# Performance work log

Measured on AMD Instinct MI355X. Metric: run time of the kernel, lower is better.

Reference implementation:

```python
import jax, jax.numpy as jnp
import numpy as np

H, N, DH, DO = 4, 4096, 128, 128   # heads, nodes, dim_hid, dim_out
ALPHA = 0.2                        # leaky-relu negative slope
NEG = -9e15                        # mask fill value (as in pyGAT)


def setup_inputs() -> dict:
    key = jax.random.key(0)
    ks = jax.random.split(key, 6)
    chems = jax.random.normal(ks[0], (H, N, DH), jnp.float32)
    adj = jax.random.randint(ks[1], (N, N), 0, 2, jnp.int32)
    s1 = 1.0 / np.sqrt(DH)
    W1 = jax.random.uniform(ks[2], (H, DH, DH), jnp.float32, -s1, s1)
    a1 = jax.random.uniform(ks[3], (H, 2 * DH), jnp.float32, -s1, s1)
    s2 = 1.0 / np.sqrt(DO)
    W2 = jax.random.uniform(ks[4], (H, H * DH, DO), jnp.float32, -s2, s2)
    a2 = jax.random.uniform(ks[5], (H, 2 * DO), jnp.float32, -s2, s2)
    return {"chems": chems, "adj": adj, "W1": W1, "a1": a1, "W2": W2, "a2": a2}


def _gat(h, W, a, mask):
    # Dense GAT layer (pyGAT style), concat=True -> elu output.
    Wh = h @ W                       # [N, d]
    d = W.shape[-1]
    src = Wh @ a[:d]                 # [N] contribution of row node
    dst = Wh @ a[d:]                 # [N] contribution of col node
    e = jax.nn.leaky_relu(src[:, None] + dst[None, :], negative_slope=ALPHA)  # [N, N]
    e = jnp.where(mask, e, NEG)
    att = jax.nn.softmax(e, axis=-1)
    return jax.nn.elu(att @ Wh)      # [N, d]


def reference(chems, adj, W1, a1, W2, a2):
    mask = adj > 0
    # stage 1: one uniform GAT head per chems[i], concat along features
    x1 = jax.vmap(_gat, in_axes=(0, 0, 0, None))(chems, W1, a1, mask)  # [H, N, DH]
    x = jnp.transpose(x1, (1, 0, 2)).reshape(N, H * DH)                # [N, H*DH]
    # stage 2: H output heads on shared x, concat along features
    x2 = jax.vmap(_gat, in_axes=(None, 0, 0, None))(x, W2, a2, mask)   # [H, N, DO]
    return jnp.transpose(x2, (1, 0, 2)).reshape(N, H * DO)             # [N, H*DO]
```

## Files before the change

### kernel.cpp

```cpp
#include <hip/hip_runtime.h>
#include <hip/hip_bf16.h>

typedef unsigned long long ull;
typedef __attribute__((ext_vector_type(8))) short short8;
typedef __attribute__((ext_vector_type(8))) unsigned short us8;
typedef __attribute__((ext_vector_type(4))) unsigned short us4;
typedef __attribute__((ext_vector_type(4))) float f32x4;

constexpr int NN = 4096;
constexpr int HH = 4;
constexpr int DD = 128;
constexpr int NW = 64;
constexpr int JSPLIT = 4;
constexpr float L2E = 1.44269504088896f;

__device__ inline unsigned short f2bf(float x) {
  unsigned u = __float_as_uint(x);
  u += 0x7FFFu + ((u >> 16) & 1u);
  return (unsigned short)(u >> 16);
}

__device__ inline short fbf(float x) {
  __bf16 b = (__bf16)x;
  short r;
  __builtin_memcpy(&r, &b, 2);
  return r;
}

__device__ inline void gload16(const void* g, void* l) {
  __builtin_amdgcn_global_load_lds(
      (const __attribute__((address_space(1))) unsigned int*)g,
      (__attribute__((address_space(3))) unsigned int*)l, 16, 0, 0);
}

__global__ __launch_bounds__(256) void pack_mask_kernel(const int* __restrict__ adj,
                                                        ull* __restrict__ mbT) {
  const int i    = blockIdx.x;
  const int lane = threadIdx.x & 63;
  const int wave = threadIdx.x >> 6;
  for (int w = wave; w < NW; w += 4) {
    int v = adj[(size_t)i * NN + w * 64 + lane];
    ull m = __ballot(v > 0);
    if (lane == 0) mbT[(size_t)w * NN + i] = m;
  }
}

__global__ __launch_bounds__(256) void cvt_bf16_kernel(const float* __restrict__ in,
                                                       unsigned short* __restrict__ out,
                                                       int n8) {
  int i = blockIdx.x * 256 + threadIdx.x;
  if (i >= n8) return;
  f32x4 a = *(const f32x4*)(in + i * 8);
  f32x4 b = *(const f32x4*)(in + i * 8 + 4);
  us8 v;
#pragma unroll
  for (int q = 0; q < 4; ++q) { v[q] = f2bf(a[q]); v[q + 4] = f2bf(b[q]); }
  *(us8*)(out + i * 8) = v;
}

__global__ __launch_bounds__(256) void prep_w_kernel(const float* __restrict__ W,
                                                     unsigned short* __restrict__ WT,
                                                     int KT) {
  int id = blockIdx.x * 256 + threadIdx.x;
  int total = HH * KT * 128 * 8;
  if (id >= total) return;
  int kc = id & 7;
  int c  = (id >> 3) & 127;
  int kt = (id >> 10) % KT;
  int h  = id / (KT * 1024);
  int K  = KT * 64;
  const float* src = W + ((size_t)h * K + kt * 64 + kc * 8) * 128 + c;
  us8 v;
#pragma unroll
  for (int e = 0; e < 8; ++e) v[e] = f2bf(src[(size_t)e * 128]);
  *(us8*)(WT + (((size_t)(h * KT + kt) * 128 + c) * 64 + ((kc ^ (c & 7)) * 8))) = v;
}

__global__ __launch_bounds__(512) void gemm_mfma_kernel(
    const unsigned short* __restrict__ A, int sA, long hsA,
    const unsigned short* __restrict__ WT, int KT,
    unsigned short* __restrict__ WhT, const float* __restrict__ avec,
    float* __restrict__ srcO, float* __restrict__ dstO) {
  __shared__ unsigned short Al[2][64 * 64];
  __shared__ unsigned short Wl[2][128 * 64];
  __shared__ float sdred[2][64][2];
  const int t   = threadIdx.x;
  const int h   = blockIdx.y;
  const int i0  = blockIdx.x * 64;
  const int l   = t & 63;
  const int wv  = t >> 6;
  const int l15 = l & 15;
  const int l16 = l >> 4;
  const int wr  = (wv >> 1) * 16;
  const int wc  = (wv & 1) * 64;
  const unsigned short* Ab = A + (size_t)h * hsA;
  const unsigned short* Wb = WT + (size_t)h * KT * 8192;

  const int arowA = wv * 8 + (l >> 3);
  const int agA   = l & 7;

  f32x4 acc[4];
#pragma unroll
  for (int cf = 0; cf < 4; ++cf) acc[cf] = (f32x4){0.f, 0.f, 0.f, 0.f};

#define G_STAGE(kt_, b_)                                                          \
  {                                                                               \
    gload16(Ab + (size_t)(i0 + arowA) * sA + (kt_) * 64 + ((agA ^ (arowA & 7)) * 8), \
            &Al[b_][(wv * 64) * 8]);                                              \
    const unsigned short* wt = Wb + (size_t)(kt_)*8192;                           \
    gload16(wt + (size_t)(wv * 64 + l) * 8, &Wl[b_][(wv * 64) * 8]);              \
    gload16(wt + (size_t)(512 + wv * 64 + l) * 8, &Wl[b_][(512 + wv * 64) * 8]);  \
  }

  G_STAGE(0, 0);
  __syncthreads();
  int buf = 0;
  for (int kt = 0; kt < KT; ++kt) {
    if (kt + 1 < KT) G_STAGE(kt + 1, buf ^ 1);
    const int arow = wr + l15;
#pragma unroll
    for (int s = 0; s < 2; ++s) {
      int kc = s * 4 + l16;
      short8 a = *(const short8*)&Al[buf][arow * 64 + ((kc ^ (arow & 7)) * 8)];
#pragma unroll
      for (int cf = 0; cf < 4; ++cf) {
        int c = wc + cf * 16 + l15;
        short8 b = *(const short8*)&Wl[buf][c * 64 + ((kc ^ (c & 7)) * 8)];
        acc[cf] = __builtin_amdgcn_mfma_f32_16x16x32_bf16(a, b, acc[cf], 0, 0, 0);
      }
    }
    __syncthreads();
    buf ^= 1;
  }

  const int wblk = i0 >> 6;
  const int g    = (wr >> 3) + (l16 >> 1);
  const int eoff = (l16 * 4) & 7;
#pragma unroll
  for (int cf = 0; cf < 4; ++cf) {
    int c = wc + cf * 16 + l15;
    us4 pk;
#pragma unroll
    for (int r = 0; r < 4; ++r) pk[r] = f2bf(acc[cf][r]);
    *(us4*)(WhT + (((size_t)(h * 64 + wblk) * 128 + c) * 64 + ((g ^ (c & 7)) * 8) + eoff)) = pk;
  }

  float ps[4] = {0.f, 0.f, 0.f, 0.f}, pd[4] = {0.f, 0.f, 0.f, 0.f};
#pragma unroll
  for (int cf = 0; cf < 4; ++cf) {
    int c = wc + cf * 16 + l15;
    float as = avec[h * 2 * DD + c];
    float ad = avec[h * 2 * DD + DD + c];
#pragma unroll
    for (int r = 0; r < 4; ++r) { ps[r] += acc[cf][r] * as; pd[r] += acc[cf][r] * ad; }
  }
#pragma unroll
  for (int off = 1; off < 16; off <<= 1) {
#pragma unroll
    for (int r = 0; r < 4; ++r) {
      ps[r] += __shfl_xor(ps[r], off, 64);
      pd[r] += __shfl_xor(pd[r], off, 64);
    }
  }
  if (l15 == 0) {
#pragma unroll
    for (int r = 0; r < 4; ++r) {
      sdred[wv & 1][wr + l16 * 4 + r][0] = ps[r];
      sdred[wv & 1][wr + l16 * 4 + r][1] = pd[r];
    }
  }
  __syncthreads();
  if (t < 128) {
    int row = t >> 1, sel = t & 1;
    float v = (sdred[0][row][sel] + sdred[1][row][sel]) * L2E;
    (sel ? dstO : srcO)[(h << 12) + i0 + row] = v;
  }
#undef G_STAGE
}

__global__ __launch_bounds__(256) void att_part_kernel(
    const unsigned short* __restrict__ WhT, const float* __restrict__ sL,
    const float* __restrict__ dL, const ull* __restrict__ mbT,
    float* __restrict__ part, float* __restrict__ sums) {
  __shared__ unsigned short whl[2][128 * 64];
  const int t   = threadIdx.x;
  const int h   = blockIdx.y;
  const int jq  = blockIdx.x & (JSPLIT - 1);
  const int i0  = (blockIdx.x / JSPLIT) * 64;
  const int l   = t & 63;
  const int wv  = t >> 6;
  const int l15 = l & 15;
  const int l16 = l >> 4;
  const int wr  = wv * 16;
  const int NIT = NW / JSPLIT;

  const int arow  = i0 + wr + l15;
  const int gr    = (h << 12) + arow;
  const float s_i = sL[gr];
  const float* dj = dL + (h << 12);
  const unsigned short* Wt = WhT + (size_t)(h * 64) * 8192;
  const int w0 = jq * NIT;

  f32x4 acc[8];
#pragma unroll
  for (int cf = 0; cf < 8; ++cf) acc[cf] = (f32x4){0.f, 0.f, 0.f, 0.f};
  float psum = 0.f;

#define A_STAGE(w_, b_)                                                    \
  {                                                                        \
    const unsigned short* gt = Wt + (size_t)(w_)*8192;                     \
    gload16(gt + (size_t)(0 * 256 + t) * 8, &whl[b_][(0 * 256 + wv * 64) * 8]); \
    gload16(gt + (size_t)(1 * 256 + t) * 8, &whl[b_][(1 * 256 + wv * 64) * 8]); \
    gload16(gt + (size_t)(2 * 256 + t) * 8, &whl[b_][(2 * 256 + wv * 64) * 8]); \
    gload16(gt + (size_t)(3 * 256 + t) * 8, &whl[b_][(3 * 256 + wv * 64) * 8]); \
  }

  A_STAGE(w0, 0);
  __syncthreads();
  int buf = 0;
  for (int it = 0; it < NIT; ++it) {
    const int w = w0 + it;
    if (it + 1 < NIT) A_STAGE(w + 1, buf ^ 1);
    ull mb = mbT[(size_t)w * NN + arow];
    short8 afr[2];
#pragma unroll
    for (int s = 0; s < 2; ++s) {
      const int bsh = s * 32 + l16 * 8;
      f32x4 d0 = *(const f32x4*)(dj + w * 64 + bsh);
      f32x4 d1 = *(const f32x4*)(dj + w * 64 + bsh + 4);
      unsigned mb8 = (unsigned)((mb >> bsh) & 0xffull);
#pragma unroll
      for (int q = 0; q < 8; ++q) {
        float tt = s_i + ((q < 4) ? d0[q] : d1[q - 4]);
        float z = fmaxf(tt, 0.2f * tt);
        z = ((mb8 >> q) & 1u) ? z : -1.0e30f;
        float pf = __builtin_amdgcn_exp2f(z);
        psum += pf;
        afr[s][q] = fbf(pf);
      }
    }
    __builtin_amdgcn_s_setprio(1);
#pragma unroll
    for (int s = 0; s < 2; ++s) {
      int kc = s * 4 + l16;
#pragma unroll
      for (int cf = 0; cf < 8; ++cf) {
        int c = cf * 16 + l15;
        short8 b = *(const short8*)&whl[buf][c * 64 + ((kc ^ (c & 7)) * 8)];
        acc[cf] = __builtin_amdgcn_mfma_f32_16x16x32_bf16(afr[s], b, acc[cf], 0, 0, 0);
      }
    }
    __builtin_amdgcn_s_setprio(0);
    __syncthreads();
    buf ^= 1;
  }
  psum += __shfl_xor(psum, 16, 64);
  psum += __shfl_xor(psum, 32, 64);
  if (l16 == 0) sums[(size_t)jq * (HH * NN) + gr] = psum;
  float* pb = part + ((size_t)jq * (HH * NN) + (h << 12) + i0) * 128;
#pragma unroll
  for (int cf = 0; cf < 8; ++cf) {
#pragma unroll
    for (int r = 0; r < 4; ++r)
      pb[(size_t)(wr + l16 * 4 + r) * 128 + cf * 16 + l15] = acc[cf][r];
  }
#undef A_STAGE
}

template <int OUTBF>
__global__ __launch_bounds__(256) void fuse_kernel(const float* __restrict__ part,
                                                   const float* __restrict__ sums,
                                                   void* __restrict__ outp) {
  int idx = blockIdx.x * 256 + threadIdx.x;
  int c4 = (idx & 31) * 4;
  int g = idx >> 5;
  int node = g & (NN - 1), h = g >> 12;
  f32x4 a = (f32x4){0.f, 0.f, 0.f, 0.f};
  float den = 0.f;
#pragma unroll
  for (int q = 0; q < JSPLIT; ++q) {
    f32x4 v = *(const f32x4*)(part + ((size_t)q * (HH * NN) + g) * 128 + c4);
#pragma unroll
    for (int r = 0; r < 4; ++r) a[r] += v[r];
    den += sums[(size_t)q * (HH * NN) + g];
  }
  float inv = 1.0f / den;
  size_t o = (size_t)node * (HH * DD) + h * DD + c4;
#pragma unroll
  for (int r = 0; r < 4; ++r) {
    float v = a[r] * inv;
    a[r] = v > 0.f ? v : __expf(v) - 1.f;
  }
  if (OUTBF) {
    us4 pk;
#pragma unroll
    for (int r = 0; r < 4; ++r) pk[r] = (unsigned short)fbf(a[r]);
    *(us4*)((unsigned short*)outp + o) = pk;
  } else {
    *(f32x4*)((float*)outp + o) = a;
  }
}

extern "C" void kernel_launch(void* const* d_in, const int* in_sizes, int n_in,
                              void* d_out, int out_size, void* d_ws, size_t ws_size,
                              hipStream_t stream) {
  const float* chems = (const float*)d_in[0];
  const int*   adj   = (const int*)d_in[1];
  const float* W1    = (const float*)d_in[2];
  const float* a1    = (const float*)d_in[3];
  const float* W2    = (const float*)d_in[4];
  const float* a2    = (const float*)d_in[5];
  float* out = (float*)d_out;

  char* p = (char*)d_ws;
  auto alloc = [&](size_t bytes) { char* r = p; p += (bytes + 255) & ~255ull; return r; };
  ull*   mbT  = (ull*)alloc((size_t)NW * NN * 8);
  unsigned short* cbf  = (unsigned short*)alloc((size_t)HH * NN * DD * 2);
  unsigned short* xbf  = (unsigned short*)alloc((size_t)NN * HH * DD * 2);
  unsigned short* WhT1 = (unsigned short*)alloc((size_t)HH * 64 * 8192 * 2);
  unsigned short* WhT2 = (unsigned short*)alloc((size_t)HH * 64 * 8192 * 2);
  unsigned short* WT1  = (unsigned short*)alloc((size_t)HH * 2 * 8192 * 2);
  unsigned short* WT2  = (unsigned short*)alloc((size_t)HH * 8 * 8192 * 2);
  float* parts = (float*)alloc((size_t)JSPLIT * HH * NN * 128 * 4);
  float* sums  = (float*)alloc((size_t)JSPLIT * HH * NN * 4);
  float* src1 = (float*)alloc((size_t)HH * NN * 4);
  float* dst1 = (float*)alloc((size_t)HH * NN * 4);
  float* src2 = (float*)alloc((size_t)HH * NN * 4);
  float* dst2 = (float*)alloc((size_t)HH * NN * 4);
  (void)ws_size; (void)in_sizes; (void)n_in; (void)out_size;

  pack_mask_kernel<<<NN, 256, 0, stream>>>(adj, mbT);
  cvt_bf16_kernel<<<(HH * NN * DD / 8 + 255) / 256, 256, 0, stream>>>(chems, cbf,
                                                                      HH * NN * DD / 8);
  prep_w_kernel<<<(HH * 2 * 1024 + 255) / 256, 256, 0, stream>>>(W1, WT1, 2);
  prep_w_kernel<<<(HH * 8 * 1024 + 255) / 256, 256, 0, stream>>>(W2, WT2, 8);

  const int FUSE_BLK = (HH * NN * DD / 4) / 256;

  gemm_mfma_kernel<<<dim3(NN / 64, HH), 512, 0, stream>>>(
      cbf, DD, (long)NN * DD, WT1, 2, WhT1, a1, src1, dst1);
  att_part_kernel<<<dim3(JSPLIT * NN / 64, HH), 256, 0, stream>>>(
      WhT1, src1, dst1, mbT, parts, sums);
  fuse_kernel<1><<<FUSE_BLK, 256, 0, stream>>>(parts, sums, xbf);
  gemm_mfma_kernel<<<dim3(NN / 64, HH), 512, 0, stream>>>(
      xbf, HH * DD, 0L, WT2, 8, WhT2, a2, src2, dst2);
  att_part_kernel<<<dim3(JSPLIT * NN / 64, HH), 256, 0, stream>>>(
      WhT2, src2, dst2, mbT, parts, sums);
  fuse_kernel<0><<<FUSE_BLK, 256, 0, stream>>>(parts, sums, out);
}
```

Measured before the change: 228.6 us.

## Factor attention exponent into per-node exps and double rows per block

Uses exp2(lrelu(s+d)) = max(e^s·e^d, e^{0.2s}·e^{0.2d}), computing the per-node exponentials once in the projection GEMM epilogue. The attention kernel then needs only multiplies and a max per pair instead of a transcendental exp. Each block now covers 128 rows, so every warp does two 16-row MFMA tiles that share the staged Wh tile. JSPLIT is raised to 8 with launch bounds set for 4 blocks, which keeps the grid size unchanged but doubles the partial-sum buffers that fuse must read. Unnormalized products could overflow or lose precision for large scores, because no max is subtracted and the exponentials are not stabilized.

```diff
diff --git a/kernel.cpp b/kernel.cpp
--- a/kernel.cpp
+++ b/kernel.cpp
@@ -11,7 +11,7 @@
 constexpr int HH = 4;
 constexpr int DD = 128;
 constexpr int NW = 64;
-constexpr int JSPLIT = 4;
+constexpr int JSPLIT = 8;
 constexpr float L2E = 1.44269504088896f;
 
 __device__ inline unsigned short f2bf(float x) {
@@ -80,7 +80,8 @@
     const unsigned short* __restrict__ A, int sA, long hsA,
     const unsigned short* __restrict__ WT, int KT,
     unsigned short* __restrict__ WhT, const float* __restrict__ avec,
-    float* __restrict__ srcO, float* __restrict__ dstO) {
+    float* __restrict__ eS, float* __restrict__ eS2,
+    float* __restrict__ eD, float* __restrict__ eD2) {
   __shared__ unsigned short Al[2][64 * 64];
   __shared__ unsigned short Wl[2][128 * 64];
   __shared__ float sdred[2][64][2];
@@ -173,38 +174,48 @@
   if (t < 128) {
     int row = t >> 1, sel = t & 1;
     float v = (sdred[0][row][sel] + sdred[1][row][sel]) * L2E;
-    (sel ? dstO : srcO)[(h << 12) + i0 + row] = v;
+    float e1 = __builtin_amdgcn_exp2f(v);
+    float e2 = __builtin_amdgcn_exp2f(0.2f * v);
+    int gg = (h << 12) + i0 + row;
+    if (sel) { eD[gg] = e1; eD2[gg] = e2; }
+    else     { eS[gg] = e1; eS2[gg] = e2; }
   }
 #undef G_STAGE
 }
 
-__global__ __launch_bounds__(256) void att_part_kernel(
-    const unsigned short* __restrict__ WhT, const float* __restrict__ sL,
-    const float* __restrict__ dL, const ull* __restrict__ mbT,
+__global__ __launch_bounds__(256, 4) void att_part_kernel(
+    const unsigned short* __restrict__ WhT, const float* __restrict__ eS,
+    const float* __restrict__ eS2, const float* __restrict__ eD,
+    const float* __restrict__ eD2, const ull* __restrict__ mbT,
     float* __restrict__ part, float* __restrict__ sums) {
   __shared__ unsigned short whl[2][128 * 64];
   const int t   = threadIdx.x;
   const int h   = blockIdx.y;
   const int jq  = blockIdx.x & (JSPLIT - 1);
-  const int i0  = (blockIdx.x / JSPLIT) * 64;
+  const int i0  = (blockIdx.x / JSPLIT) * 128;
   const int l   = t & 63;
   const int wv  = t >> 6;
   const int l15 = l & 15;
   const int l16 = l >> 4;
-  const int wr  = wv * 16;
+  const int wr  = wv * 32;
   const int NIT = NW / JSPLIT;
 
-  const int arow  = i0 + wr + l15;
-  const int gr    = (h << 12) + arow;
-  const float s_i = sL[gr];
-  const float* dj = dL + (h << 12);
+  const int r0  = i0 + wr + l15;
+  const int g0  = (h << 12) + r0;
+  const float es0 = eS[g0],      es0b = eS2[g0];
+  const float es1 = eS[g0 + 16], es1b = eS2[g0 + 16];
+  const float* pD  = eD  + (h << 12);
+  const float* pD2 = eD2 + (h << 12);
   const unsigned short* Wt = WhT + (size_t)(h * 64) * 8192;
   const int w0 = jq * NIT;
 
-  f32x4 acc[8];
-#pragma unroll
-  for (int cf = 0; cf < 8; ++cf) acc[cf] = (f32x4){0.f, 0.f, 0.f, 0.f};
-  float psum = 0.f;
+  f32x4 acc0[8], acc1[8];
+#pragma unroll
+  for (int cf = 0; cf < 8; ++cf) {
+    acc0[cf] = (f32x4){0.f, 0.f, 0.f, 0.f};
+    acc1[cf] = (f32x4){0.f, 0.f, 0.f, 0.f};
+  }
+  float ps0 = 0.f, ps1 = 0.f;
 
 #define A_STAGE(w_, b_)                                                    \
   {                                                                        \
@@ -221,22 +232,30 @@
   for (int it = 0; it < NIT; ++it) {
     const int w = w0 + it;
     if (it + 1 < NIT) A_STAGE(w + 1, buf ^ 1);
-    ull mb = mbT[(size_t)w * NN + arow];
-    short8 afr[2];
+    ull mb0 = mbT[(size_t)w * NN + r0];
+    ull mb1 = mbT[(size_t)w * NN + r0 + 16];
+    short8 a0[2], a1[2];
 #pragma unroll
     for (int s = 0; s < 2; ++s) {
       const int bsh = s * 32 + l16 * 8;
-      f32x4 d0 = *(const f32x4*)(dj + w * 64 + bsh);
-      f32x4 d1 = *(const f32x4*)(dj + w * 64 + bsh + 4);
-      unsigned mb8 = (unsigned)((mb >> bsh) & 0xffull);
+      f32x4 dA  = *(const f32x4*)(pD  + w * 64 + bsh);
+      f32x4 dB  = *(const f32x4*)(pD  + w * 64 + bsh + 4);
+      f32x4 d2A = *(const f32x4*)(pD2 + w * 64 + bsh);
+      f32x4 d2B = *(const f32x4*)(pD2 + w * 64 + bsh + 4);
+      unsigned m0 = (unsigned)((mb0 >> bsh) & 0xffull);
+      unsigned m1 = (unsigned)((mb1 >> bsh) & 0xffull);
 #pragma unroll
       for (int q = 0; q < 8; ++q) {
-        float tt = s_i + ((q < 4) ? d0[q] : d1[q - 4]);
-        float z = fmaxf(tt, 0.2f * tt);
-        z = ((mb8 >> q) & 1u) ? z : -1.0e30f;
-        float pf = __builtin_amdgcn_exp2f(z);
-        psum += pf;
-        afr[s][q] = fbf(pf);
+        float ed  = (q < 4) ? dA[q] : dB[q - 4];
+        float ed2 = (q < 4) ? d2A[q] : d2B[q - 4];
+        float p0 = fmaxf(es0 * ed, es0b * ed2);
+        p0 = ((m0 >> q) & 1u) ? p0 : 0.f;
+        ps0 += p0;
+        a0[s][q] = fbf(p0);
+        float p1 = fmaxf(es1 * ed, es1b * ed2);
+        p1 = ((m1 >> q) & 1u) ? p1 : 0.f;
+        ps1 += p1;
+        a1[s][q] = fbf(p1);
       }
     }
     __builtin_amdgcn_s_setprio(1);
@@ -247,22 +266,30 @@
       for (int cf = 0; cf < 8; ++cf) {
         int c = cf * 16 + l15;
         short8 b = *(const short8*)&whl[buf][c * 64 + ((kc ^ (c & 7)) * 8)];
-        acc[cf] = __builtin_amdgcn_mfma_f32_16x16x32_bf16(afr[s], b, acc[cf], 0, 0, 0);
+        acc0[cf] = __builtin_amdgcn_mfma_f32_16x16x32_bf16(a0[s], b, acc0[cf], 0, 0, 0);
+        acc1[cf] = __builtin_amdgcn_mfma_f32_16x16x32_bf16(a1[s], b, acc1[cf], 0, 0, 0);
       }
     }
     __builtin_amdgcn_s_setprio(0);
     __syncthreads();
     buf ^= 1;
   }
-  psum += __shfl_xor(psum, 16, 64);
-  psum += __shfl_xor(psum, 32, 64);
-  if (l16 == 0) sums[(size_t)jq * (HH * NN) + gr] = psum;
+  ps0 += __shfl_xor(ps0, 16, 64);
+  ps0 += __shfl_xor(ps0, 32, 64);
+  ps1 += __shfl_xor(ps1, 16, 64);
+  ps1 += __shfl_xor(ps1, 32, 64);
+  if (l16 == 0) {
+    sums[(size_t)jq * (HH * NN) + g0] = ps0;
+    sums[(size_t)jq * (HH * NN) + g0 + 16] = ps1;
+  }
   float* pb = part + ((size_t)jq * (HH * NN) + (h << 12) + i0) * 128;
 #pragma unroll
   for (int cf = 0; cf < 8; ++cf) {
 #pragma unroll
-    for (int r = 0; r < 4; ++r)
-      pb[(size_t)(wr + l16 * 4 + r) * 128 + cf * 16 + l15] = acc[cf][r];
+    for (int r = 0; r < 4; ++r) {
+      pb[(size_t)(wr + l16 * 4 + r) * 128 + cf * 16 + l15] = acc0[cf][r];
+      pb[(size_t)(wr + 16 + l16 * 4 + r) * 128 + cf * 16 + l15] = acc1[cf][r];
+    }
   }
 #undef A_STAGE
 }
@@ -323,10 +350,14 @@
   unsigned short* WT2  = (unsigned short*)alloc((size_t)HH * 8 * 8192 * 2);
   float* parts = (float*)alloc((size_t)JSPLIT * HH * NN * 128 * 4);
   float* sums  = (float*)alloc((size_t)JSPLIT * HH * NN * 4);
-  float* src1 = (float*)alloc((size_t)HH * NN * 4);
-  float* dst1 = (float*)alloc((size_t)HH * NN * 4);
-  float* src2 = (float*)alloc((size_t)HH * NN * 4);
-  float* dst2 = (float*)alloc((size_t)HH * NN * 4);
+  float* eS1  = (float*)alloc((size_t)HH * NN * 4);
+  float* eS1b = (float*)alloc((size_t)HH * NN * 4);
+  float* eD1  = (float*)alloc((size_t)HH * NN * 4);
+  float* eD1b = (float*)alloc((size_t)HH * NN * 4);
+  float* eS2  = (float*)alloc((size_t)HH * NN * 4);
+  float* eS2b = (float*)alloc((size_t)HH * NN * 4);
+  float* eD2  = (float*)alloc((size_t)HH * NN * 4);
+  float* eD2b = (float*)alloc((size_t)HH * NN * 4);
   (void)ws_size; (void)in_sizes; (void)n_in; (void)out_size;
 
   pack_mask_kernel<<<NN, 256, 0, stream>>>(adj, mbT);
@@ -338,13 +369,13 @@
   const int FUSE_BLK = (HH * NN * DD / 4) / 256;
 
   gemm_mfma_kernel<<<dim3(NN / 64, HH), 512, 0, stream>>>(
-      cbf, DD, (long)NN * DD, WT1, 2, WhT1, a1, src1, dst1);
-  att_part_kernel<<<dim3(JSPLIT * NN / 64, HH), 256, 0, stream>>>(
-      WhT1, src1, dst1, mbT, parts, sums);
+      cbf, DD, (long)NN * DD, WT1, 2, WhT1, a1, eS1, eS1b, eD1, eD1b);
+  att_part_kernel<<<dim3(JSPLIT * NN / 128, HH), 256, 0, stream>>>(
+      WhT1, eS1, eS1b, eD1, eD1b, mbT, parts, sums);
   fuse_kernel<1><<<FUSE_BLK, 256, 0, stream>>>(parts, sums, xbf);
   gemm_mfma_kernel<<<dim3(NN / 64, HH), 512, 0, stream>>>(
-      xbf, HH * DD, 0L, WT2, 8, WhT2, a2, src2, dst2);
-  att_part_kernel<<<dim3(JSPLIT * NN / 64, HH), 256, 0, stream>>>(
-      WhT2, src2, dst2, mbT, parts, sums);
+      xbf, HH * DD, 0L, WT2, 8, WhT2, a2, eS2, eS2b, eD2, eD2b);
+  att_part_kernel<<<dim3(JSPLIT * NN / 128, HH), 256, 0, stream>>>(
+      WhT2, eS2, eS2b, eD2, eD2b, mbT, parts, sums);
   fuse_kernel<0><<<FUSE_BLK, 256, 0, stream>>>(parts, sums, out);
 }
```

Result: slower. 239.7 us (+4.9%).
